# Performance work log

Hardware: AMD Instinct MI355X
Metric: run time of the kernel (lower is better)

## Reference

```python
import jax, jax.numpy as jnp
import numpy as np

B, CIN, COUT, COFF, H, W = 4, 256, 256, 256, 64, 64
DG, K = 16, 3            # deformable groups, kernel size
KK = K * K               # 9 taps


def _conv3x3(x, w, b):
    y = jax.lax.conv_general_dilated(x, w, window_strides=(1, 1), padding='SAME',
                                     dimension_numbers=('NCHW', 'OIHW', 'NCHW'))
    return y + b[None, :, None, None]


def _bilinear_sample(xg, ys, xs):
    # xg: [B,DG,Cg,H,W]; ys,xs: [B,DG,Ho,Wo] float sampling coords (zero padding outside)
    Bn, dg, Cg, Hh, Ww = xg.shape
    xf = xg.reshape(Bn, dg, Cg, Hh * Ww)
    y0 = jnp.floor(ys)
    x0 = jnp.floor(xs)
    wy = (ys - y0)[:, :, None]  # [B,DG,1,Ho,Wo]
    wx = (xs - x0)[:, :, None]

    def gather(yi, xi):
        valid = (yi >= 0) & (yi < Hh) & (xi >= 0) & (xi < Ww)
        yc = jnp.clip(yi, 0, Hh - 1).astype(jnp.int32)
        xc = jnp.clip(xi, 0, Ww - 1).astype(jnp.int32)
        idx = (yc * Ww + xc).reshape(Bn, dg, 1, -1)
        v = jnp.take_along_axis(xf, jnp.broadcast_to(idx, (Bn, dg, Cg, idx.shape[-1])), axis=-1)
        v = v.reshape(Bn, dg, Cg, ys.shape[2], ys.shape[3])
        return v * valid[:, :, None].astype(xg.dtype)

    v00 = gather(y0, x0)
    v01 = gather(y0, x0 + 1)
    v10 = gather(y0 + 1, x0)
    v11 = gather(y0 + 1, x0 + 1)
    return v00 * (1 - wy) * (1 - wx) + v01 * (1 - wy) * wx + v10 * wy * (1 - wx) + v11 * wy * wx


def _deform_conv2d(x, offset, mask, weight, bias):
    # torchvision modulated deform_conv2d, stride=1, padding=1, dilation=1, groups=1
    Bn, C, Hh, Ww = x.shape
    Cg = C // DG
    xg = x.reshape(Bn, DG, Cg, Hh, Ww)
    # offset channel layout: 2*(g*KK + k) -> dy, +1 -> dx
    off = offset.reshape(Bn, DG, KK, 2, Hh, Ww)
    msk = mask.reshape(Bn, DG, KK, Hh, Ww)
    wk = weight.reshape(weight.shape[0], DG, Cg, K, K)
    hb = jnp.arange(Hh, dtype=x.dtype)[:, None]
    wb = jnp.arange(Ww, dtype=x.dtype)[None, :]
    acc = jnp.zeros((Bn, weight.shape[0], Hh, Ww), dtype=x.dtype)
    for ki in range(K):
        for kj in range(K):
            k = ki * K + kj
            ys = hb - 1 + ki + off[:, :, k, 0]   # padding=1, dilation=1
            xs = wb - 1 + kj + off[:, :, k, 1]
            s = _bilinear_sample(xg, ys, xs) * msk[:, :, k][:, :, None]  # [B,DG,Cg,H,W]
            acc = acc + jnp.einsum('bgchw,ogc->bohw', s, wk[:, :, :, ki, kj])
    return acc + bias[None, :, None, None]


def setup_inputs() -> dict:
    key = jax.random.key(0)
    ks = jax.random.split(key, 10)
    s = 0.02
    return {
        'x': jax.random.normal(ks[0], (B, CIN, H, W), jnp.float32),
        'offset_feat': jax.random.normal(ks[1], (B, COFF, H, W), jnp.float32),
        'weight': jax.random.normal(ks[2], (COUT, CIN, K, K), jnp.float32) * s,
        'bias': jax.random.normal(ks[3], (COUT,), jnp.float32) * s,
        'w1': jax.random.normal(ks[4], (COUT, COFF, K, K), jnp.float32) * s,
        'b1': jax.random.normal(ks[5], (COUT,), jnp.float32) * s,
        'w2': jax.random.normal(ks[6], (COUT, COUT, K, K), jnp.float32) * s,
        'b2': jax.random.normal(ks[7], (COUT,), jnp.float32) * s,
        'w3': jax.random.normal(ks[8], (27 * DG, COUT, K, K), jnp.float32) * 0.01,
        'b3': jax.random.normal(ks[9], (27 * DG,), jnp.float32) * 0.01,
    }


def reference(x, offset_feat, weight, bias, w1, b1, w2, b2, w3, b3):
    out = jax.nn.silu(_conv3x3(offset_feat, w1, b1))
    out = jax.nn.silu(_conv3x3(out, w2, b2))
    out = _conv3x3(out, w3, b3)                 # [B, 27*DG, H, W]
    o1, o2, m = jnp.split(out, 3, axis=1)
    offset = jnp.concatenate([o1, o2], axis=1)  # [B, 2*DG*9, H, W]
    mask = jax.nn.sigmoid(m)                    # [B, DG*9, H, W]
    return _deform_conv2d(x, offset, mask, weight, bias)
```

## Files before the change

### kernel.cpp

```cpp
#include <hip/hip_runtime.h>
#include <math.h>

typedef __attribute__((ext_vector_type(8))) short  bf16x8;
typedef __attribute__((ext_vector_type(8))) unsigned short u16x8;
typedef __attribute__((ext_vector_type(4))) float  f32x4;

#define MTOT 16384

__device__ __forceinline__ float b2f(unsigned short h) {
  return __uint_as_float(((unsigned int)h) << 16);
}
__device__ __forceinline__ unsigned short f2bf(float f) {
  unsigned int u = __float_as_uint(f);
  unsigned int r = (u + 0x7fffu + ((u >> 16) & 1u)) >> 16;
  return (unsigned short)r;
}
__device__ __forceinline__ void gload16(const unsigned short* g, unsigned short* l) {
  __builtin_amdgcn_global_load_lds(
      (const __attribute__((address_space(1))) void*)g,
      (__attribute__((address_space(3))) void*)l, 16, 0, 0);
}

__global__ __launch_bounds__(256) void nhwc_kernel(const float* __restrict__ in,
                                                   unsigned short* __restrict__ out) {
  const int y = blockIdx.x, b = blockIdx.y;
  const int t = threadIdx.x;
  __shared__ float lds[64 * 65];
  for (int c0 = 0; c0 < 256; c0 += 64) {
    #pragma unroll
    for (int i = 0; i < 16; ++i) {
      int cl = i * 4 + (t >> 6);
      int xx = t & 63;
      lds[cl * 65 + xx] = in[(((size_t)b * 256 + c0 + cl) * 64 + y) * 64 + xx];
    }
    __syncthreads();
    const int plane = c0 >> 6;
    #pragma unroll
    for (int i = 0; i < 16; ++i) {
      int xx = i * 4 + (t >> 6);
      int cl = t & 63;
      int m  = (b << 12) + (y << 6) + xx;
      out[((size_t)plane * MTOT + m) * 64 + cl] = f2bf(lds[cl * 65 + xx]);
    }
    __syncthreads();
  }
}

__global__ __launch_bounds__(256) void wprep_kernel(const float* __restrict__ w,
                                                    unsigned short* __restrict__ Wp,
                                                    int NPAD, int COUT_valid) {
  const int kkc4 = blockIdx.x;
  const int kk = kkc4 >> 2, c4 = kkc4 & 3;
  const int co = blockIdx.y * 4 + (threadIdx.x >> 6);
  const int c16 = threadIdx.x & 63;
  float v = (co < COUT_valid) ? w[((size_t)co * 256 + c4 * 64 + c16) * 9 + kk] : 0.0f;
  Wp[((size_t)kkc4 * NPAD + co) * 64 + c16] = f2bf(v);
}

__global__ __launch_bounds__(256) void sampler_kernel(const float* __restrict__ t3,
                                                      const unsigned short* __restrict__ xh,
                                                      unsigned short* __restrict__ S) {
  const int t = threadIdx.x;
  const int g = t & 15;
  const int m = blockIdx.x * 16 + (t >> 4);
  const int b = m >> 12, pix = m & 4095, y = pix >> 6, x = pix & 63;
  const float* off = t3 + (size_t)m * 432;
  const size_t gbase = ((size_t)(g >> 2) * MTOT + ((size_t)b << 12)) * 64 + (g & 3) * 16;

  #pragma unroll
  for (int kk = 0; kk < 9; ++kk) {
    const int ki = kk / 3, kj = kk % 3;
    float dyv = off[2 * (g * 9 + kk)];
    float dxv = off[2 * (g * 9 + kk) + 1];
    float ml  = off[288 + g * 9 + kk];
    float mk  = 1.0f / (1.0f + __expf(-ml));
    float ysf = (float)(y - 1 + ki) + dyv;
    float xsf = (float)(x - 1 + kj) + dxv;
    float y0f = floorf(ysf), x0f = floorf(xsf);
    float wy = ysf - y0f, wx = xsf - x0f;
    int yi0 = (int)y0f, xi0 = (int)x0f;
    int yi1 = yi0 + 1, xi1 = xi0 + 1;
    bool vy0 = (yi0 >= 0) && (yi0 < 64), vy1 = (yi1 >= 0) && (yi1 < 64);
    bool vx0 = (xi0 >= 0) && (xi0 < 64), vx1 = (xi1 >= 0) && (xi1 < 64);
    int yc0 = min(max(yi0, 0), 63), yc1 = min(max(yi1, 0), 63);
    int xc0 = min(max(xi0, 0), 63), xc1 = min(max(xi1, 0), 63);
    float w00 = (vy0 && vx0) ? (1.f - wy) * (1.f - wx) * mk : 0.f;
    float w01 = (vy0 && vx1) ? (1.f - wy) * wx * mk : 0.f;
    float w10 = (vy1 && vx0) ? wy * (1.f - wx) * mk : 0.f;
    float w11 = (vy1 && vx1) ? wy * wx * mk : 0.f;

    float sacc[16];
    #pragma unroll
    for (int c = 0; c < 16; ++c) sacc[c] = 0.f;

    const int p00 = yc0 * 64 + xc0, p01 = yc0 * 64 + xc1;
    const int p10 = yc1 * 64 + xc0, p11 = yc1 * 64 + xc1;
    {
      u16x8 lo = *(const u16x8*)(xh + gbase + (size_t)p00 * 64);
      u16x8 hi = *(const u16x8*)(xh + gbase + (size_t)p00 * 64 + 8);
      #pragma unroll
      for (int j = 0; j < 8; ++j) { sacc[j] += w00 * b2f(lo[j]); sacc[8 + j] += w00 * b2f(hi[j]); }
    }
    {
      u16x8 lo = *(const u16x8*)(xh + gbase + (size_t)p01 * 64);
      u16x8 hi = *(const u16x8*)(xh + gbase + (size_t)p01 * 64 + 8);
      #pragma unroll
      for (int j = 0; j < 8; ++j) { sacc[j] += w01 * b2f(lo[j]); sacc[8 + j] += w01 * b2f(hi[j]); }
    }
    {
      u16x8 lo = *(const u16x8*)(xh + gbase + (size_t)p10 * 64);
      u16x8 hi = *(const u16x8*)(xh + gbase + (size_t)p10 * 64 + 8);
      #pragma unroll
      for (int j = 0; j < 8; ++j) { sacc[j] += w10 * b2f(lo[j]); sacc[8 + j] += w10 * b2f(hi[j]); }
    }
    {
      u16x8 lo = *(const u16x8*)(xh + gbase + (size_t)p11 * 64);
      u16x8 hi = *(const u16x8*)(xh + gbase + (size_t)p11 * 64 + 8);
      #pragma unroll
      for (int j = 0; j < 8; ++j) { sacc[j] += w11 * b2f(lo[j]); sacc[8 + j] += w11 * b2f(hi[j]); }
    }
    u16x8 olo, ohi;
    #pragma unroll
    for (int j = 0; j < 8; ++j) { olo[j] = f2bf(sacc[j]); ohi[j] = f2bf(sacc[8 + j]); }
    unsigned short* sp = S + ((size_t)(kk * 4 + (g >> 2)) * MTOT + m) * 64 + (g & 3) * 16;
    *(u16x8*)sp = olo;
    *(u16x8*)(sp + 8) = ohi;
  }
}

template<int NPAD, int EPI, bool IMPLICIT>
__global__ __launch_bounds__(512, 1) void gemm8_kernel(
    const unsigned short* __restrict__ A,
    const unsigned short* __restrict__ W,
    const float* __restrict__ bias,
    void* __restrict__ outp,
    const unsigned short* __restrict__ zbuf,
    int Nvalid) {
  constexpr int BM = 128, BN = 128, BK = 64;
  constexpr int NSTEP = 36;
  constexpr int BUFE = (BM + BN) * BK;
  __shared__ unsigned short lds[2][BUFE];

  const int t = threadIdx.x, lane = t & 63, w = t >> 6;
  const int wm = w >> 2, wn = w & 3;
  const int m0 = blockIdx.x * BM, n0 = blockIdx.y * BN;

  const unsigned short* baseA[2];
  const unsigned short* zsrcA[2];
  unsigned int vmaskA[2];
  #pragma unroll
  for (int i = 0; i < 2; ++i) {
    int c   = (i * 8 + w) * 64 + lane;
    int row = c >> 3;
    int ccl = (c & 7) ^ (row & 7);
    int m   = m0 + row;
    baseA[i] = A + (size_t)m * 64 + ccl * 8;
    zsrcA[i] = zbuf + ccl * 8;
    if (IMPLICIT) {
      int y = (m >> 6) & 63, x = m & 63;
      unsigned int vm = 0;
      #pragma unroll
      for (int kk = 0; kk < 9; ++kk) {
        int dy = kk / 3 - 1, dx = kk % 3 - 1;
        if ((unsigned)(y + dy) < 64u && (unsigned)(x + dx) < 64u) vm |= (1u << kk);
      }
      vmaskA[i] = vm;
    } else {
      vmaskA[i] = 0;
    }
  }
  const unsigned short* baseB[2];
  #pragma unroll
  for (int j = 0; j < 2; ++j) {
    int c   = (j * 8 + w) * 64 + lane;
    int row = c >> 3;
    int ccl = (c & 7) ^ (row & 7);
    baseB[j] = W + (size_t)(n0 + row) * 64 + ccl * 8;
  }

  int offA[4][2], offB[2][2];
  #pragma unroll
  for (int mi = 0; mi < 4; ++mi) {
    int r = wm * 64 + mi * 16 + (lane & 15);
    #pragma unroll
    for (int kh = 0; kh < 2; ++kh) {
      int ccl = kh * 4 + (lane >> 4);
      offA[mi][kh] = r * 64 + ((ccl ^ (r & 7)) * 8);
    }
  }
  #pragma unroll
  for (int nj = 0; nj < 2; ++nj) {
    int r = wn * 32 + nj * 16 + (lane & 15);
    #pragma unroll
    for (int kh = 0; kh < 2; ++kh) {
      int ccl = kh * 4 + (lane >> 4);
      offB[nj][kh] = BM * BK + r * 64 + ((ccl ^ (r & 7)) * 8);
    }
  }

  f32x4 acc[4][2];
  #pragma unroll
  for (int mi = 0; mi < 4; ++mi)
    #pragma unroll
    for (int nj = 0; nj < 2; ++nj) acc[mi][nj] = (f32x4){0.f, 0.f, 0.f, 0.f};

  auto STAGE = [&](int sn, unsigned short* buf) {
    const long boff = (long)sn * (NPAD * 64);
    if (IMPLICIT) {
      int kkn = sn >> 2;
      int q3  = kkn / 3;
      int dy = q3 - 1, dx = kkn - q3 * 3 - 1;
      const long aoff = (long)(sn & 3) * (MTOT * 64) + (long)(dy * 64 + dx) * 64;
      #pragma unroll
      for (int i = 0; i < 2; ++i) {
        const unsigned short* src = ((vmaskA[i] >> kkn) & 1u) ? baseA[i] + aoff : zsrcA[i];
        gload16(src, buf + (i * 8 + w) * 512);
      }
    } else {
      const long aoff = (long)sn * (MTOT * 64);
      #pragma unroll
      for (int i = 0; i < 2; ++i)
        gload16(baseA[i] + aoff, buf + (i * 8 + w) * 512);
    }
    #pragma unroll
    for (int j = 0; j < 2; ++j)
      gload16(baseB[j] + boff, buf + BM * BK + (j * 8 + w) * 512);
  };

  STAGE(0, lds[0]);

  for (int s = 0; s < NSTEP; ++s) {
    if (s + 1 < NSTEP) {
      STAGE(s + 1, lds[(s + 1) & 1]);
      asm volatile("s_waitcnt vmcnt(4)" ::: "memory");
    } else {
      asm volatile("s_waitcnt vmcnt(0)" ::: "memory");
    }
    __builtin_amdgcn_s_barrier();
    __builtin_amdgcn_sched_barrier(0);

    const unsigned short* cb = lds[s & 1];
    bf16x8 af[4][2], bfg[2][2];
    #pragma unroll
    for (int mi = 0; mi < 4; ++mi)
      #pragma unroll
      for (int kh = 0; kh < 2; ++kh)
        af[mi][kh] = *(const bf16x8*)&cb[offA[mi][kh]];
    #pragma unroll
    for (int nj = 0; nj < 2; ++nj)
      #pragma unroll
      for (int kh = 0; kh < 2; ++kh)
        bfg[nj][kh] = *(const bf16x8*)&cb[offB[nj][kh]];

    #pragma unroll
    for (int kh = 0; kh < 2; ++kh)
      #pragma unroll
      for (int mi = 0; mi < 4; ++mi)
        #pragma unroll
        for (int nj = 0; nj < 2; ++nj)
          acc[mi][nj] = __builtin_amdgcn_mfma_f32_16x16x32_bf16(af[mi][kh], bfg[nj][kh],
                                                                acc[mi][nj], 0, 0, 0);
    __builtin_amdgcn_sched_barrier(0);
    asm volatile("s_waitcnt lgkmcnt(0)" ::: "memory");
    __builtin_amdgcn_s_barrier();
  }

  const int gmBase = m0 + wm * 64 + (lane >> 4) * 4;
  const int gnBase = n0 + wn * 32 + (lane & 15);
  #pragma unroll
  for (int nj = 0; nj < 2; ++nj) {
    const int gn = gnBase + nj * 16;
    const float bv = (gn < Nvalid) ? bias[gn] : 0.f;
    #pragma unroll
    for (int mi = 0; mi < 4; ++mi) {
      #pragma unroll
      for (int r = 0; r < 4; ++r) {
        const int gm = gmBase + mi * 16 + r;
        float v = acc[mi][nj][r] + bv;
        if (EPI == 0) {
          float sv = v / (1.0f + __expf(-v));
          ((unsigned short*)outp)[((size_t)(gn >> 6) * MTOT + gm) * 64 + (gn & 63)] = f2bf(sv);
        } else if (EPI == 1) {
          if (gn < Nvalid) ((float*)outp)[(size_t)gm * 432 + gn] = v;
        } else {
          ((float*)outp)[((size_t)(gm >> 12) * 256 + gn) * 4096 + (gm & 4095)] = v;
        }
      }
    }
  }
}

extern "C" void kernel_launch(void* const* d_in, const int* in_sizes, int n_in,
                              void* d_out, int out_size, void* d_ws, size_t ws_size,
                              hipStream_t stream) {
  const float* x      = (const float*)d_in[0];
  const float* offeat = (const float*)d_in[1];
  const float* weight = (const float*)d_in[2];
  const float* bias   = (const float*)d_in[3];
  const float* w1     = (const float*)d_in[4];
  const float* b1     = (const float*)d_in[5];
  const float* w2     = (const float*)d_in[6];
  const float* b2     = (const float*)d_in[7];
  const float* w3     = (const float*)d_in[8];
  const float* b3     = (const float*)d_in[9];
  float* out = (float*)d_out;

  char* ws = (char*)d_ws;
  unsigned short* xh  = (unsigned short*)(ws + 0);
  float*          t3  = (float*)(ws + 8388608);
  unsigned short* Wd  = (unsigned short*)(ws + 36700160);
  unsigned short* zb  = (unsigned short*)(ws + 37879808);
  unsigned short* S   = (unsigned short*)(ws + 37880064);
  unsigned short* fh  = (unsigned short*)(ws + 37880064);
  unsigned short* t1  = (unsigned short*)(ws + 46268672);
  unsigned short* t2  = (unsigned short*)(ws + 54657280);
  unsigned short* W1p = (unsigned short*)(ws + 63045888);
  unsigned short* W2p = (unsigned short*)(ws + 64225536);
  unsigned short* W3p = (unsigned short*)(ws + 65405184);

  hipMemsetAsync(zb, 0, 256, stream);

  nhwc_kernel<<<dim3(64, 4), 256, 0, stream>>>(x, xh);
  nhwc_kernel<<<dim3(64, 4), 256, 0, stream>>>(offeat, fh);
  wprep_kernel<<<dim3(36, 64), 256, 0, stream>>>(w1, W1p, 256, 256);
  wprep_kernel<<<dim3(36, 64), 256, 0, stream>>>(w2, W2p, 256, 256);
  wprep_kernel<<<dim3(36, 128), 256, 0, stream>>>(w3, W3p, 512, 432);
  wprep_kernel<<<dim3(36, 64), 256, 0, stream>>>(weight, Wd, 256, 256);

  gemm8_kernel<256, 0, true><<<dim3(128, 2), 512, 0, stream>>>(fh, W1p, b1, t1, zb, 256);
  gemm8_kernel<256, 0, true><<<dim3(128, 2), 512, 0, stream>>>(t1, W2p, b2, t2, zb, 256);

  gemm8_kernel<512, 1, true><<<dim3(128, 4), 512, 0, stream>>>(t2, W3p, b3, t3, zb, 432);

  sampler_kernel<<<dim3(1024), 256, 0, stream>>>(t3, xh, S);

  gemm8_kernel<256, 2, false><<<dim3(128, 2), 512, 0, stream>>>(S, Wd, bias, out, zb, 256);
}
```

Before: 196.3 us.

## Fuse deformable bilinear sampler into final GEMM producer loop

Removes the standalone sampler kernel and its S intermediate buffer. The final GEMM now gathers the bilinear samples directly into the LDS A tiles, software-pipelined against the MFMA work of the previous K-step. This avoids writing and re-reading the large sampled bf16 tensor and saves one launch. In exchange, the gathers are recomputed for each of the two N-blocks, and gather latency now sits inside the GEMM loop, where it may stall the MFMA pipeline.

```diff
diff --git a/kernel.cpp b/kernel.cpp
--- a/kernel.cpp
+++ b/kernel.cpp
@@ -55,77 +55,6 @@
   const int c16 = threadIdx.x & 63;
   float v = (co < COUT_valid) ? w[((size_t)co * 256 + c4 * 64 + c16) * 9 + kk] : 0.0f;
   Wp[((size_t)kkc4 * NPAD + co) * 64 + c16] = f2bf(v);
-}
-
-__global__ __launch_bounds__(256) void sampler_kernel(const float* __restrict__ t3,
-                                                      const unsigned short* __restrict__ xh,
-                                                      unsigned short* __restrict__ S) {
-  const int t = threadIdx.x;
-  const int g = t & 15;
-  const int m = blockIdx.x * 16 + (t >> 4);
-  const int b = m >> 12, pix = m & 4095, y = pix >> 6, x = pix & 63;
-  const float* off = t3 + (size_t)m * 432;
-  const size_t gbase = ((size_t)(g >> 2) * MTOT + ((size_t)b << 12)) * 64 + (g & 3) * 16;
-
-  #pragma unroll
-  for (int kk = 0; kk < 9; ++kk) {
-    const int ki = kk / 3, kj = kk % 3;
-    float dyv = off[2 * (g * 9 + kk)];
-    float dxv = off[2 * (g * 9 + kk) + 1];
-    float ml  = off[288 + g * 9 + kk];
-    float mk  = 1.0f / (1.0f + __expf(-ml));
-    float ysf = (float)(y - 1 + ki) + dyv;
-    float xsf = (float)(x - 1 + kj) + dxv;
-    float y0f = floorf(ysf), x0f = floorf(xsf);
-    float wy = ysf - y0f, wx = xsf - x0f;
-    int yi0 = (int)y0f, xi0 = (int)x0f;
-    int yi1 = yi0 + 1, xi1 = xi0 + 1;
-    bool vy0 = (yi0 >= 0) && (yi0 < 64), vy1 = (yi1 >= 0) && (yi1 < 64);
-    bool vx0 = (xi0 >= 0) && (xi0 < 64), vx1 = (xi1 >= 0) && (xi1 < 64);
-    int yc0 = min(max(yi0, 0), 63), yc1 = min(max(yi1, 0), 63);
-    int xc0 = min(max(xi0, 0), 63), xc1 = min(max(xi1, 0), 63);
-    float w00 = (vy0 && vx0) ? (1.f - wy) * (1.f - wx) * mk : 0.f;
-    float w01 = (vy0 && vx1) ? (1.f - wy) * wx * mk : 0.f;
-    float w10 = (vy1 && vx0) ? wy * (1.f - wx) * mk : 0.f;
-    float w11 = (vy1 && vx1) ? wy * wx * mk : 0.f;
-
-    float sacc[16];
-    #pragma unroll
-    for (int c = 0; c < 16; ++c) sacc[c] = 0.f;
-
-    const int p00 = yc0 * 64 + xc0, p01 = yc0 * 64 + xc1;
-    const int p10 = yc1 * 64 + xc0, p11 = yc1 * 64 + xc1;
-    {
-      u16x8 lo = *(const u16x8*)(xh + gbase + (size_t)p00 * 64);
-      u16x8 hi = *(const u16x8*)(xh + gbase + (size_t)p00 * 64 + 8);
-      #pragma unroll
-      for (int j = 0; j < 8; ++j) { sacc[j] += w00 * b2f(lo[j]); sacc[8 + j] += w00 * b2f(hi[j]); }
-    }
-    {
-      u16x8 lo = *(const u16x8*)(xh + gbase + (size_t)p01 * 64);
-      u16x8 hi = *(const u16x8*)(xh + gbase + (size_t)p01 * 64 + 8);
-      #pragma unroll
-      for (int j = 0; j < 8; ++j) { sacc[j] += w01 * b2f(lo[j]); sacc[8 + j] += w01 * b2f(hi[j]); }
-    }
-    {
-      u16x8 lo = *(const u16x8*)(xh + gbase + (size_t)p10 * 64);
-      u16x8 hi = *(const u16x8*)(xh + gbase + (size_t)p10 * 64 + 8);
-      #pragma unroll
-      for (int j = 0; j < 8; ++j) { sacc[j] += w10 * b2f(lo[j]); sacc[8 + j] += w10 * b2f(hi[j]); }
-    }
-    {
-      u16x8 lo = *(const u16x8*)(xh + gbase + (size_t)p11 * 64);
-      u16x8 hi = *(const u16x8*)(xh + gbase + (size_t)p11 * 64 + 8);
-      #pragma unroll
-      for (int j = 0; j < 8; ++j) { sacc[j] += w11 * b2f(lo[j]); sacc[8 + j] += w11 * b2f(hi[j]); }
-    }
-    u16x8 olo, ohi;
-    #pragma unroll
-    for (int j = 0; j < 8; ++j) { olo[j] = f2bf(sacc[j]); ohi[j] = f2bf(sacc[8 + j]); }
-    unsigned short* sp = S + ((size_t)(kk * 4 + (g >> 2)) * MTOT + m) * 64 + (g & 3) * 16;
-    *(u16x8*)sp = olo;
-    *(u16x8*)(sp + 8) = ohi;
-  }
 }
 
 template<int NPAD, int EPI, bool IMPLICIT>
@@ -280,11 +209,196 @@
         if (EPI == 0) {
           float sv = v / (1.0f + __expf(-v));
           ((unsigned short*)outp)[((size_t)(gn >> 6) * MTOT + gm) * 64 + (gn & 63)] = f2bf(sv);
-        } else if (EPI == 1) {
+        } else {
           if (gn < Nvalid) ((float*)outp)[(size_t)gm * 432 + gn] = v;
-        } else {
-          ((float*)outp)[((size_t)(gm >> 12) * 256 + gn) * 4096 + (gm & 4095)] = v;
         }
+      }
+    }
+  }
+}
+
+__global__ __launch_bounds__(512, 1) void deform_fused_kernel(
+    const float* __restrict__ t3,
+    const unsigned short* __restrict__ xh,
+    const unsigned short* __restrict__ W,
+    const float* __restrict__ bias,
+    float* __restrict__ out) {
+  constexpr int BM = 128, BN = 128, BK = 64;
+  constexpr int NSTEP = 36;
+  __shared__ unsigned short ldsA[2][BM * BK];
+  __shared__ unsigned short ldsB[2][BN * BK];
+
+  const int t = threadIdx.x, lane = t & 63, w = t >> 6;
+  const int wm = w >> 2, wn = w & 3;
+  const int m0 = blockIdx.x * BM, n0 = blockIdx.y * BN;
+
+  const int mr = t >> 2, q = t & 3;
+  const int gms = m0 + mr;
+  const int bs = gms >> 12, pix = gms & 4095;
+  const int ysi = pix >> 6, xsi = pix & 63;
+  const float* offp = t3 + (size_t)gms * 432;
+  const int wofA0 = mr * 64 + (((2 * q)     ^ (mr & 7)) * 8);
+  const int wofA1 = mr * 64 + (((2 * q + 1) ^ (mr & 7)) * 8);
+
+  const unsigned short* baseB[2];
+  int wofB[2];
+  #pragma unroll
+  for (int j = 0; j < 2; ++j) {
+    int c   = (j * 8 + w) * 64 + lane;
+    int row = c >> 3;
+    int ccl = (c & 7) ^ (row & 7);
+    baseB[j] = W + (size_t)(n0 + row) * 64 + ccl * 8;
+    wofB[j]  = (j * 8 + w) * 512;
+  }
+
+  int offA[4][2], offB[2][2];
+  #pragma unroll
+  for (int mi = 0; mi < 4; ++mi) {
+    int r = wm * 64 + mi * 16 + (lane & 15);
+    #pragma unroll
+    for (int kh = 0; kh < 2; ++kh) {
+      int ccl = kh * 4 + (lane >> 4);
+      offA[mi][kh] = r * 64 + ((ccl ^ (r & 7)) * 8);
+    }
+  }
+  #pragma unroll
+  for (int nj = 0; nj < 2; ++nj) {
+    int r = wn * 32 + nj * 16 + (lane & 15);
+    #pragma unroll
+    for (int kh = 0; kh < 2; ++kh) {
+      int ccl = kh * 4 + (lane >> 4);
+      offB[nj][kh] = r * 64 + ((ccl ^ (r & 7)) * 8);
+    }
+  }
+
+  f32x4 acc[4][2];
+  #pragma unroll
+  for (int mi = 0; mi < 4; ++mi)
+    #pragma unroll
+    for (int nj = 0; nj < 2; ++nj) acc[mi][nj] = (f32x4){0.f, 0.f, 0.f, 0.f};
+
+  auto T_LOAD = [&](int sn, float& dyv, float& dxv, float& ml) {
+    int kk = sn >> 2;
+    int g  = ((sn & 3) << 2) + q;
+    int base = g * 9 + kk;
+    dyv = offp[2 * base];
+    dxv = offp[2 * base + 1];
+    ml  = offp[288 + base];
+  };
+
+  auto GATHER = [&](int sn, float dyv, float dxv, float ml, u16x8* cr, f32x4& wg) {
+    int kk = sn >> 2;
+    int ki = kk / 3, kj = kk - 3 * (kk / 3);
+    float mk = 1.0f / (1.0f + __expf(-ml));
+    float ysf = (float)(ysi - 1 + ki) + dyv;
+    float xsf = (float)(xsi - 1 + kj) + dxv;
+    float y0f = floorf(ysf), x0f = floorf(xsf);
+    float wy = ysf - y0f, wx = xsf - x0f;
+    int yi0 = (int)y0f, xi0 = (int)x0f;
+    int yi1 = yi0 + 1, xi1 = xi0 + 1;
+    bool vy0 = (yi0 >= 0) && (yi0 < 64), vy1 = (yi1 >= 0) && (yi1 < 64);
+    bool vx0 = (xi0 >= 0) && (xi0 < 64), vx1 = (xi1 >= 0) && (xi1 < 64);
+    int yc0 = min(max(yi0, 0), 63), yc1 = min(max(yi1, 0), 63);
+    int xc0 = min(max(xi0, 0), 63), xc1 = min(max(xi1, 0), 63);
+    wg[0] = (vy0 && vx0) ? (1.f - wy) * (1.f - wx) * mk : 0.f;
+    wg[1] = (vy0 && vx1) ? (1.f - wy) * wx * mk : 0.f;
+    wg[2] = (vy1 && vx0) ? wy * (1.f - wx) * mk : 0.f;
+    wg[3] = (vy1 && vx1) ? wy * wx * mk : 0.f;
+    const unsigned short* gb = xh + ((size_t)(sn & 3) * MTOT + ((size_t)bs << 12)) * 64 + q * 16;
+    const int p00 = yc0 * 64 + xc0, p01 = yc0 * 64 + xc1;
+    const int p10 = yc1 * 64 + xc0, p11 = yc1 * 64 + xc1;
+    cr[0] = *(const u16x8*)(gb + (size_t)p00 * 64);
+    cr[1] = *(const u16x8*)(gb + (size_t)p00 * 64 + 8);
+    cr[2] = *(const u16x8*)(gb + (size_t)p01 * 64);
+    cr[3] = *(const u16x8*)(gb + (size_t)p01 * 64 + 8);
+    cr[4] = *(const u16x8*)(gb + (size_t)p10 * 64);
+    cr[5] = *(const u16x8*)(gb + (size_t)p10 * 64 + 8);
+    cr[6] = *(const u16x8*)(gb + (size_t)p11 * 64);
+    cr[7] = *(const u16x8*)(gb + (size_t)p11 * 64 + 8);
+  };
+
+  auto COMBINE_WRITE = [&](const u16x8* cr, f32x4 wg, unsigned short* bufA) {
+    u16x8 olo, ohi;
+    #pragma unroll
+    for (int j = 0; j < 8; ++j) {
+      float sl = wg[0] * b2f(cr[0][j]) + wg[1] * b2f(cr[2][j])
+               + wg[2] * b2f(cr[4][j]) + wg[3] * b2f(cr[6][j]);
+      float sh = wg[0] * b2f(cr[1][j]) + wg[1] * b2f(cr[3][j])
+               + wg[2] * b2f(cr[5][j]) + wg[3] * b2f(cr[7][j]);
+      olo[j] = f2bf(sl);
+      ohi[j] = f2bf(sh);
+    }
+    *(u16x8*)&bufA[wofA0] = olo;
+    *(u16x8*)&bufA[wofA1] = ohi;
+  };
+
+  {
+    float dy0, dx0, ml0;
+    T_LOAD(0, dy0, dx0, ml0);
+    u16x8 cr[8]; f32x4 wg;
+    GATHER(0, dy0, dx0, ml0, cr, wg);
+    COMBINE_WRITE(cr, wg, ldsA[0]);
+    #pragma unroll
+    for (int j = 0; j < 2; ++j)
+      gload16(baseB[j], ldsB[0] + wofB[j]);
+  }
+  __syncthreads();
+
+  float dyN, dxN, mlN;
+  T_LOAD(1, dyN, dxN, mlN);
+
+  for (int s = 0; s < NSTEP; ++s) {
+    const int sn = s + 1;
+    u16x8 cr[8]; f32x4 wg;
+    if (sn < NSTEP) {
+      #pragma unroll
+      for (int j = 0; j < 2; ++j)
+        gload16(baseB[j] + (size_t)sn * (256 * 64), ldsB[sn & 1] + wofB[j]);
+      GATHER(sn, dyN, dxN, mlN, cr, wg);
+    }
+    float dy2 = 0.f, dx2 = 0.f, ml2 = 0.f;
+    if (s + 2 < NSTEP) T_LOAD(s + 2, dy2, dx2, ml2);
+
+    const unsigned short* cA = ldsA[s & 1];
+    const unsigned short* cB = ldsB[s & 1];
+    bf16x8 af[4][2], bfg[2][2];
+    #pragma unroll
+    for (int mi = 0; mi < 4; ++mi)
+      #pragma unroll
+      for (int kh = 0; kh < 2; ++kh)
+        af[mi][kh] = *(const bf16x8*)&cA[offA[mi][kh]];
+    #pragma unroll
+    for (int nj = 0; nj < 2; ++nj)
+      #pragma unroll
+      for (int kh = 0; kh < 2; ++kh)
+        bfg[nj][kh] = *(const bf16x8*)&cB[offB[nj][kh]];
+
+    #pragma unroll
+    for (int kh = 0; kh < 2; ++kh)
+      #pragma unroll
+      for (int mi = 0; mi < 4; ++mi)
+        #pragma unroll
+        for (int nj = 0; nj < 2; ++nj)
+          acc[mi][nj] = __builtin_amdgcn_mfma_f32_16x16x32_bf16(af[mi][kh], bfg[nj][kh],
+                                                                acc[mi][nj], 0, 0, 0);
+
+    if (sn < NSTEP) COMBINE_WRITE(cr, wg, ldsA[sn & 1]);
+    dyN = dy2; dxN = dx2; mlN = ml2;
+    __syncthreads();
+  }
+
+  const int gmBase = m0 + wm * 64 + (lane >> 4) * 4;
+  const int gnBase = n0 + wn * 32 + (lane & 15);
+  #pragma unroll
+  for (int nj = 0; nj < 2; ++nj) {
+    const int gn = gnBase + nj * 16;
+    const float bv = bias[gn];
+    #pragma unroll
+    for (int mi = 0; mi < 4; ++mi) {
+      #pragma unroll
+      for (int r = 0; r < 4; ++r) {
+        const int gm = gmBase + mi * 16 + r;
+        out[((size_t)(gm >> 12) * 256 + gn) * 4096 + (gm & 4095)] = acc[mi][nj][r] + bv;
       }
     }
   }
@@ -310,7 +424,6 @@
   float*          t3  = (float*)(ws + 8388608);
   unsigned short* Wd  = (unsigned short*)(ws + 36700160);
   unsigned short* zb  = (unsigned short*)(ws + 37879808);
-  unsigned short* S   = (unsigned short*)(ws + 37880064);
   unsigned short* fh  = (unsigned short*)(ws + 37880064);
   unsigned short* t1  = (unsigned short*)(ws + 46268672);
   unsigned short* t2  = (unsigned short*)(ws + 54657280);
@@ -332,7 +445,5 @@
 
   gemm8_kernel<512, 1, true><<<dim3(128, 4), 512, 0, stream>>>(t2, W3p, b3, t3, zb, 432);
 
-  sampler_kernel<<<dim3(1024), 256, 0, stream>>>(t3, xh, S);
-
-  gemm8_kernel<256, 2, false><<<dim3(128, 2), 512, 0, stream>>>(S, Wd, bias, out, zb, 256);
-}
+  deform_fused_kernel<<<dim3(128, 2), 512, 0, stream>>>(t3, xh, Wd, bias, out);
+}
```

Result: slower. 222.5 us (+13.4%).

## Shrink GEMM N-tile to 64, trim offset-conv padding, split sampler channels per thread

Applied to the files above, without the earlier changes.

Three of the four GEMMs (conv2, the offset/mask conv, and the final deform GEMM) now use a 128x64 tile instead of 128x128. This doubles the block count from 256 to 512 (896 for the offset conv) so more CUs are busy on a 256-CU part, with launch bounds allowing several blocks per CU. The offset conv's padded N drops from 512 to 448, which removes 64 padded output columns of wasted MFMA work. The sampler now gives each thread 8 channels instead of 16, doubling its thread count and cutting per-thread registers. The trade-off is lower operand reuse per block and more redundant sigmoid/coordinate math per thread.

```diff
diff --git a/kernel.cpp b/kernel.cpp
--- a/kernel.cpp
+++ b/kernel.cpp
@@ -61,11 +61,12 @@
                                                       const unsigned short* __restrict__ xh,
                                                       unsigned short* __restrict__ S) {
   const int t = threadIdx.x;
-  const int g = t & 15;
-  const int m = blockIdx.x * 16 + (t >> 4);
+  const int h = t & 1;
+  const int g = (t >> 1) & 15;
+  const int m = blockIdx.x * 8 + (t >> 5);
   const int b = m >> 12, pix = m & 4095, y = pix >> 6, x = pix & 63;
   const float* off = t3 + (size_t)m * 432;
-  const size_t gbase = ((size_t)(g >> 2) * MTOT + ((size_t)b << 12)) * 64 + (g & 3) * 16;
+  const size_t gbase = ((size_t)(g >> 2) * MTOT + ((size_t)b << 12)) * 64 + (g & 3) * 16 + h * 8;
 
   #pragma unroll
   for (int kk = 0; kk < 9; ++kk) {
@@ -89,60 +90,171 @@
     float w10 = (vy1 && vx0) ? wy * (1.f - wx) * mk : 0.f;
     float w11 = (vy1 && vx1) ? wy * wx * mk : 0.f;
 
-    float sacc[16];
-    #pragma unroll
-    for (int c = 0; c < 16; ++c) sacc[c] = 0.f;
-
     const int p00 = yc0 * 64 + xc0, p01 = yc0 * 64 + xc1;
     const int p10 = yc1 * 64 + xc0, p11 = yc1 * 64 + xc1;
-    {
-      u16x8 lo = *(const u16x8*)(xh + gbase + (size_t)p00 * 64);
-      u16x8 hi = *(const u16x8*)(xh + gbase + (size_t)p00 * 64 + 8);
-      #pragma unroll
-      for (int j = 0; j < 8; ++j) { sacc[j] += w00 * b2f(lo[j]); sacc[8 + j] += w00 * b2f(hi[j]); }
-    }
-    {
-      u16x8 lo = *(const u16x8*)(xh + gbase + (size_t)p01 * 64);
-      u16x8 hi = *(const u16x8*)(xh + gbase + (size_t)p01 * 64 + 8);
-      #pragma unroll
-      for (int j = 0; j < 8; ++j) { sacc[j] += w01 * b2f(lo[j]); sacc[8 + j] += w01 * b2f(hi[j]); }
-    }
-    {
-      u16x8 lo = *(const u16x8*)(xh + gbase + (size_t)p10 * 64);
-      u16x8 hi = *(const u16x8*)(xh + gbase + (size_t)p10 * 64 + 8);
-      #pragma unroll
-      for (int j = 0; j < 8; ++j) { sacc[j] += w10 * b2f(lo[j]); sacc[8 + j] += w10 * b2f(hi[j]); }
-    }
-    {
-      u16x8 lo = *(const u16x8*)(xh + gbase + (size_t)p11 * 64);
-      u16x8 hi = *(const u16x8*)(xh + gbase + (size_t)p11 * 64 + 8);
-      #pragma unroll
-      for (int j = 0; j < 8; ++j) { sacc[j] += w11 * b2f(lo[j]); sacc[8 + j] += w11 * b2f(hi[j]); }
-    }
-    u16x8 olo, ohi;
-    #pragma unroll
-    for (int j = 0; j < 8; ++j) { olo[j] = f2bf(sacc[j]); ohi[j] = f2bf(sacc[8 + j]); }
-    unsigned short* sp = S + ((size_t)(kk * 4 + (g >> 2)) * MTOT + m) * 64 + (g & 3) * 16;
-    *(u16x8*)sp = olo;
-    *(u16x8*)(sp + 8) = ohi;
+    u16x8 c00 = *(const u16x8*)(xh + gbase + (size_t)p00 * 64);
+    u16x8 c01 = *(const u16x8*)(xh + gbase + (size_t)p01 * 64);
+    u16x8 c10 = *(const u16x8*)(xh + gbase + (size_t)p10 * 64);
+    u16x8 c11 = *(const u16x8*)(xh + gbase + (size_t)p11 * 64);
+    u16x8 o;
+    #pragma unroll
+    for (int j = 0; j < 8; ++j) {
+      float s = w00 * b2f(c00[j]) + w01 * b2f(c01[j]) + w10 * b2f(c10[j]) + w11 * b2f(c11[j]);
+      o[j] = f2bf(s);
+    }
+    *(u16x8*)(S + ((size_t)(kk * 4 + (g >> 2)) * MTOT + m) * 64 + (g & 3) * 16 + h * 8) = o;
+  }
+}
+
+__global__ __launch_bounds__(512, 1) void convA_kernel(
+    const unsigned short* __restrict__ A,
+    const unsigned short* __restrict__ W,
+    const float* __restrict__ bias,
+    unsigned short* __restrict__ outp,
+    const unsigned short* __restrict__ zbuf) {
+  constexpr int BM = 128, BN = 128, BK = 64, NSTEP = 36, NPAD = 256;
+  __shared__ unsigned short lds[2][(BM + BN) * BK];
+
+  const int t = threadIdx.x, lane = t & 63, w = t >> 6;
+  const int wm = w >> 2, wn = w & 3;
+  const int m0 = blockIdx.x * BM, n0 = blockIdx.y * BN;
+
+  const unsigned short* baseA[2];
+  const unsigned short* zsrcA[2];
+  unsigned int vmaskA[2];
+  #pragma unroll
+  for (int i = 0; i < 2; ++i) {
+    int c   = (i * 8 + w) * 64 + lane;
+    int row = c >> 3;
+    int ccl = (c & 7) ^ (row & 7);
+    int m   = m0 + row;
+    baseA[i] = A + (size_t)m * 64 + ccl * 8;
+    zsrcA[i] = zbuf + ccl * 8;
+    int y = (m >> 6) & 63, x = m & 63;
+    unsigned int vm = 0;
+    #pragma unroll
+    for (int kk = 0; kk < 9; ++kk) {
+      int dy = kk / 3 - 1, dx = kk % 3 - 1;
+      if ((unsigned)(y + dy) < 64u && (unsigned)(x + dx) < 64u) vm |= (1u << kk);
+    }
+    vmaskA[i] = vm;
+  }
+  const unsigned short* baseB[2];
+  #pragma unroll
+  for (int j = 0; j < 2; ++j) {
+    int c   = (j * 8 + w) * 64 + lane;
+    int row = c >> 3;
+    int ccl = (c & 7) ^ (row & 7);
+    baseB[j] = W + (size_t)(n0 + row) * 64 + ccl * 8;
+  }
+
+  int offA[4][2], offB[2][2];
+  #pragma unroll
+  for (int mi = 0; mi < 4; ++mi) {
+    int r = wm * 64 + mi * 16 + (lane & 15);
+    #pragma unroll
+    for (int kh = 0; kh < 2; ++kh)
+      offA[mi][kh] = r * 64 + (((kh * 4 + (lane >> 4)) ^ (r & 7)) * 8);
+  }
+  #pragma unroll
+  for (int nj = 0; nj < 2; ++nj) {
+    int r = wn * 32 + nj * 16 + (lane & 15);
+    #pragma unroll
+    for (int kh = 0; kh < 2; ++kh)
+      offB[nj][kh] = BM * BK + r * 64 + (((kh * 4 + (lane >> 4)) ^ (r & 7)) * 8);
+  }
+
+  f32x4 acc[4][2];
+  #pragma unroll
+  for (int mi = 0; mi < 4; ++mi)
+    #pragma unroll
+    for (int nj = 0; nj < 2; ++nj) acc[mi][nj] = (f32x4){0.f, 0.f, 0.f, 0.f};
+
+  auto STAGE = [&](int sn, unsigned short* buf) {
+    int kkn = sn >> 2;
+    int q3  = kkn / 3;
+    const long aoff = (long)(sn & 3) * (MTOT * 64) + (long)((q3 - 1) * 64 + (kkn - q3 * 3 - 1)) * 64;
+    const long boff = (long)sn * (NPAD * 64);
+    #pragma unroll
+    for (int i = 0; i < 2; ++i) {
+      const unsigned short* src = ((vmaskA[i] >> kkn) & 1u) ? baseA[i] + aoff : zsrcA[i];
+      gload16(src, buf + (i * 8 + w) * 512);
+    }
+    #pragma unroll
+    for (int j = 0; j < 2; ++j)
+      gload16(baseB[j] + boff, buf + BM * BK + (j * 8 + w) * 512);
+  };
+
+  STAGE(0, lds[0]);
+
+  for (int s = 0; s < NSTEP; ++s) {
+    if (s + 1 < NSTEP) {
+      STAGE(s + 1, lds[(s + 1) & 1]);
+      asm volatile("s_waitcnt vmcnt(4)" ::: "memory");
+    } else {
+      asm volatile("s_waitcnt vmcnt(0)" ::: "memory");
+    }
+    __builtin_amdgcn_s_barrier();
+    __builtin_amdgcn_sched_barrier(0);
+
+    const unsigned short* cb = lds[s & 1];
+    bf16x8 af[4][2], bfg[2][2];
+    #pragma unroll
+    for (int mi = 0; mi < 4; ++mi)
+      #pragma unroll
+      for (int kh = 0; kh < 2; ++kh)
+        af[mi][kh] = *(const bf16x8*)&cb[offA[mi][kh]];
+    #pragma unroll
+    for (int nj = 0; nj < 2; ++nj)
+      #pragma unroll
+      for (int kh = 0; kh < 2; ++kh)
+        bfg[nj][kh] = *(const bf16x8*)&cb[offB[nj][kh]];
+
+    #pragma unroll
+    for (int kh = 0; kh < 2; ++kh)
+      #pragma unroll
+      for (int mi = 0; mi < 4; ++mi)
+        #pragma unroll
+        for (int nj = 0; nj < 2; ++nj)
+          acc[mi][nj] = __builtin_amdgcn_mfma_f32_16x16x32_bf16(af[mi][kh], bfg[nj][kh],
+                                                                acc[mi][nj], 0, 0, 0);
+    __builtin_amdgcn_sched_barrier(0);
+    asm volatile("s_waitcnt lgkmcnt(0)" ::: "memory");
+    __builtin_amdgcn_s_barrier();
+  }
+
+  const int gmBase = m0 + wm * 64 + (lane >> 4) * 4;
+  const int gnBase = n0 + wn * 32 + (lane & 15);
+  #pragma unroll
+  for (int nj = 0; nj < 2; ++nj) {
+    const int gn = gnBase + nj * 16;
+    const float bv = bias[gn];
+    #pragma unroll
+    for (int mi = 0; mi < 4; ++mi) {
+      #pragma unroll
+      for (int r = 0; r < 4; ++r) {
+        const int gm = gmBase + mi * 16 + r;
+        float v = acc[mi][nj][r] + bv;
+        float sv = v / (1.0f + __expf(-v));
+        outp[((size_t)(gn >> 6) * MTOT + gm) * 64 + (gn & 63)] = f2bf(sv);
+      }
+    }
   }
 }
 
 template<int NPAD, int EPI, bool IMPLICIT>
-__global__ __launch_bounds__(512, 1) void gemm8_kernel(
+__global__ __launch_bounds__(512, 4) void gemmB_kernel(
     const unsigned short* __restrict__ A,
     const unsigned short* __restrict__ W,
     const float* __restrict__ bias,
     void* __restrict__ outp,
     const unsigned short* __restrict__ zbuf,
     int Nvalid) {
-  constexpr int BM = 128, BN = 128, BK = 64;
-  constexpr int NSTEP = 36;
-  constexpr int BUFE = (BM + BN) * BK;
-  __shared__ unsigned short lds[2][BUFE];
+  constexpr int BM = 128, BN = 64, BK = 64, NSTEP = 36;
+  __shared__ unsigned short lds[2][(BM + BN) * BK];
 
   const int t = threadIdx.x, lane = t & 63, w = t >> 6;
-  const int wm = w >> 2, wn = w & 3;
+  const int wm = w >> 1, wn = w & 1;
   const int m0 = blockIdx.x * BM, n0 = blockIdx.y * BN;
 
   const unsigned short* baseA[2];
@@ -169,38 +281,33 @@
       vmaskA[i] = 0;
     }
   }
-  const unsigned short* baseB[2];
-  #pragma unroll
-  for (int j = 0; j < 2; ++j) {
-    int c   = (j * 8 + w) * 64 + lane;
+  const unsigned short* baseB;
+  {
+    int c   = w * 64 + lane;
     int row = c >> 3;
     int ccl = (c & 7) ^ (row & 7);
-    baseB[j] = W + (size_t)(n0 + row) * 64 + ccl * 8;
-  }
-
-  int offA[4][2], offB[2][2];
-  #pragma unroll
-  for (int mi = 0; mi < 4; ++mi) {
-    int r = wm * 64 + mi * 16 + (lane & 15);
-    #pragma unroll
-    for (int kh = 0; kh < 2; ++kh) {
-      int ccl = kh * 4 + (lane >> 4);
-      offA[mi][kh] = r * 64 + ((ccl ^ (r & 7)) * 8);
-    }
+    baseB = W + (size_t)(n0 + row) * 64 + ccl * 8;
+  }
+
+  int offA[2][2], offB[2][2];
+  #pragma unroll
+  for (int mi = 0; mi < 2; ++mi) {
+    int r = wm * 32 + mi * 16 + (lane & 15);
+    #pragma unroll
+    for (int kh = 0; kh < 2; ++kh)
+      offA[mi][kh] = r * 64 + (((kh * 4 + (lane >> 4)) ^ (r & 7)) * 8);
   }
   #pragma unroll
   for (int nj = 0; nj < 2; ++nj) {
     int r = wn * 32 + nj * 16 + (lane & 15);
     #pragma unroll
-    for (int kh = 0; kh < 2; ++kh) {
-      int ccl = kh * 4 + (lane >> 4);
-      offB[nj][kh] = BM * BK + r * 64 + ((ccl ^ (r & 7)) * 8);
-    }
-  }
-
-  f32x4 acc[4][2];
-  #pragma unroll
-  for (int mi = 0; mi < 4; ++mi)
+    for (int kh = 0; kh < 2; ++kh)
+      offB[nj][kh] = BM * BK + r * 64 + (((kh * 4 + (lane >> 4)) ^ (r & 7)) * 8);
+  }
+
+  f32x4 acc[2][2];
+  #pragma unroll
+  for (int mi = 0; mi < 2; ++mi)
     #pragma unroll
     for (int nj = 0; nj < 2; ++nj) acc[mi][nj] = (f32x4){0.f, 0.f, 0.f, 0.f};
 
@@ -209,8 +316,7 @@
     if (IMPLICIT) {
       int kkn = sn >> 2;
       int q3  = kkn / 3;
-      int dy = q3 - 1, dx = kkn - q3 * 3 - 1;
-      const long aoff = (long)(sn & 3) * (MTOT * 64) + (long)(dy * 64 + dx) * 64;
+      const long aoff = (long)(sn & 3) * (MTOT * 64) + (long)((q3 - 1) * 64 + (kkn - q3 * 3 - 1)) * 64;
       #pragma unroll
       for (int i = 0; i < 2; ++i) {
         const unsigned short* src = ((vmaskA[i] >> kkn) & 1u) ? baseA[i] + aoff : zsrcA[i];
@@ -222,9 +328,7 @@
       for (int i = 0; i < 2; ++i)
         gload16(baseA[i] + aoff, buf + (i * 8 + w) * 512);
     }
-    #pragma unroll
-    for (int j = 0; j < 2; ++j)
-      gload16(baseB[j] + boff, buf + BM * BK + (j * 8 + w) * 512);
+    gload16(baseB + boff, buf + BM * BK + w * 512);
   };
 
   STAGE(0, lds[0]);
@@ -232,7 +336,7 @@
   for (int s = 0; s < NSTEP; ++s) {
     if (s + 1 < NSTEP) {
       STAGE(s + 1, lds[(s + 1) & 1]);
-      asm volatile("s_waitcnt vmcnt(4)" ::: "memory");
+      asm volatile("s_waitcnt vmcnt(3)" ::: "memory");
     } else {
       asm volatile("s_waitcnt vmcnt(0)" ::: "memory");
     }
@@ -240,9 +344,9 @@
     __builtin_amdgcn_sched_barrier(0);
 
     const unsigned short* cb = lds[s & 1];
-    bf16x8 af[4][2], bfg[2][2];
-    #pragma unroll
-    for (int mi = 0; mi < 4; ++mi)
+    bf16x8 af[2][2], bfg[2][2];
+    #pragma unroll
+    for (int mi = 0; mi < 2; ++mi)
       #pragma unroll
       for (int kh = 0; kh < 2; ++kh)
         af[mi][kh] = *(const bf16x8*)&cb[offA[mi][kh]];
@@ -255,7 +359,7 @@
     #pragma unroll
     for (int kh = 0; kh < 2; ++kh)
       #pragma unroll
-      for (int mi = 0; mi < 4; ++mi)
+      for (int mi = 0; mi < 2; ++mi)
         #pragma unroll
         for (int nj = 0; nj < 2; ++nj)
           acc[mi][nj] = __builtin_amdgcn_mfma_f32_16x16x32_bf16(af[mi][kh], bfg[nj][kh],
@@ -265,14 +369,14 @@
     __builtin_amdgcn_s_barrier();
   }
 
-  const int gmBase = m0 + wm * 64 + (lane >> 4) * 4;
+  const int gmBase = m0 + wm * 32 + (lane >> 4) * 4;
   const int gnBase = n0 + wn * 32 + (lane & 15);
   #pragma unroll
   for (int nj = 0; nj < 2; ++nj) {
     const int gn = gnBase + nj * 16;
     const float bv = (gn < Nvalid) ? bias[gn] : 0.f;
     #pragma unroll
-    for (int mi = 0; mi < 4; ++mi) {
+    for (int mi = 0; mi < 2; ++mi) {
       #pragma unroll
       for (int r = 0; r < 4; ++r) {
         const int gm = gmBase + mi * 16 + r;
@@ -324,15 +428,14 @@
   nhwc_kernel<<<dim3(64, 4), 256, 0, stream>>>(offeat, fh);
   wprep_kernel<<<dim3(36, 64), 256, 0, stream>>>(w1, W1p, 256, 256);
   wprep_kernel<<<dim3(36, 64), 256, 0, stream>>>(w2, W2p, 256, 256);
-  wprep_kernel<<<dim3(36, 128), 256, 0, stream>>>(w3, W3p, 512, 432);
+  wprep_kernel<<<dim3(36, 112), 256, 0, stream>>>(w3, W3p, 448, 432);
   wprep_kernel<<<dim3(36, 64), 256, 0, stream>>>(weight, Wd, 256, 256);
 
-  gemm8_kernel<256, 0, true><<<dim3(128, 2), 512, 0, stream>>>(fh, W1p, b1, t1, zb, 256);
-  gemm8_kernel<256, 0, true><<<dim3(128, 2), 512, 0, stream>>>(t1, W2p, b2, t2, zb, 256);
-
-  gemm8_kernel<512, 1, true><<<dim3(128, 4), 512, 0, stream>>>(t2, W3p, b3, t3, zb, 432);
-
-  sampler_kernel<<<dim3(1024), 256, 0, stream>>>(t3, xh, S);
-
-  gemm8_kernel<256, 2, false><<<dim3(128, 2), 512, 0, stream>>>(S, Wd, bias, out, zb, 256);
-}
+  convA_kernel<<<dim3(128, 2), 512, 0, stream>>>(fh, W1p, b1, t1, zb);
+  gemmB_kernel<256, 0, true><<<dim3(128, 4), 512, 0, stream>>>(t1, W2p, b2, t2, zb, 256);
+  gemmB_kernel<448, 1, true><<<dim3(128, 7), 512, 0, stream>>>(t2, W3p, b3, t3, zb, 432);
+
+  sampler_kernel<<<dim3(2048), 256, 0, stream>>>(t3, xh, S);
+
+  gemmB_kernel<256, 2, false><<<dim3(128, 4), 512, 0, stream>>>(S, Wd, bias, out, zb, 256);
+}
```

Result: slower. 203.1 us (+3.5%).
